# Kernel optimization log

Hardware: AMD Instinct MI355X
Metric: run time of the kernel (lower is better)

The kernel has to match this reference:

```python
import jax, jax.numpy as jnp
import numpy as np

EPS = 1e-5
NUM_HEADS = 4


def setup_inputs() -> dict:
    key = jax.random.key(0)
    ks = jax.random.split(key, 6)
    B, C, H, W = 16, 256, 32, 32
    x = jax.random.normal(ks[0], (B, C, H, W), dtype=jnp.float32)
    gamma = jnp.ones((C,), jnp.float32)
    beta = jnp.zeros((C,), jnp.float32)
    run_mean = jax.random.normal(ks[1], (C,), dtype=jnp.float32) * 0.1
    run_var = jax.random.uniform(ks[2], (C,), dtype=jnp.float32, minval=0.5, maxval=1.5)
    qkv_w = jax.random.normal(ks[3], (3 * C, C), dtype=jnp.float32) * (1.0 / np.sqrt(C))
    qkv_b = jnp.zeros((3 * C,), jnp.float32)
    out_w = jax.random.normal(ks[4], (C, C), dtype=jnp.float32) * (1.0 / np.sqrt(C))
    out_b = jnp.zeros((C,), jnp.float32)
    return {"x": x, "gamma": gamma, "beta": beta, "run_mean": run_mean,
            "run_var": run_var, "qkv_w": qkv_w, "qkv_b": qkv_b,
            "out_w": out_w, "out_b": out_b}


def reference(x, gamma, beta, run_mean, run_var, qkv_w, qkv_b, out_w, out_b):
    B, C, H, W = x.shape
    n = NUM_HEADS
    hd = C // n
    # BatchNorm2d (eval mode, running stats)
    inv = jax.lax.rsqrt(run_var + EPS)
    xn = (x - run_mean[:, None, None]) * (inv * gamma)[:, None, None] + beta[:, None, None]
    # 1x1 conv -> QKV: [B, 3C, H, W]
    qkv = jnp.einsum('oc,bchw->bohw', qkv_w, xn) + qkv_b[:, None, None]
    qkv = qkv.reshape(B, n, 3 * hd, H, W)
    q, k, v = qkv[:, :, :hd], qkv[:, :, hd:2 * hd], qkv[:, :, 2 * hd:]
    # full spatial attention; note scale is sqrt(C), per source
    attn = jnp.einsum('bnchw,bncyx->bnhwyx', q, k) / jnp.sqrt(jnp.float32(C))
    attn = jax.nn.softmax(attn.reshape(B, n, H, W, H * W), axis=-1)
    attn = attn.reshape(B, n, H, W, H, W)
    av = jnp.einsum('bnhwyx,bncyx->bnchw', attn, v).reshape(B, C, H, W)
    out = jnp.einsum('oc,bchw->bohw', out_w, av) + out_b[:, None, None]
    return x + out
```

## Files before the change

kernel.cpp:

```cpp
#include <hip/hip_runtime.h>
#include <hip/hip_bf16.h>

__device__ __forceinline__ float bf2f(unsigned short u) {
    return __uint_as_float(((unsigned int)u) << 16);
}
__device__ __forceinline__ unsigned short f2bf(float f) {
    unsigned int u = __float_as_uint(f);
    unsigned int r = (u + 0x7fffu + ((u >> 16) & 1u)) >> 16;
    return (unsigned short)r;
}
__device__ __forceinline__ float ld1(const void* p, long i, bool isf32) {
    return isf32 ? ((const float*)p)[i] : bf2f(((const unsigned short*)p)[i]);
}

typedef __attribute__((ext_vector_type(8))) short bh8;
typedef __attribute__((ext_vector_type(4))) float f32x4;

#define S_TOK 1024
#define C_DIM 256
#define O_QKV 768
#define HD    64
#define NREG  196608
#define QOFF  0
#define KOFF  65536
#define VOFF  131072

__global__ __launch_bounds__(256) void prep_kernel(
    const void* __restrict__ gamma, const void* __restrict__ beta,
    const void* __restrict__ rmean, const void* __restrict__ rvar,
    const void* __restrict__ qkv_w, const void* __restrict__ qkv_b,
    const void* __restrict__ out_w, const void* __restrict__ out_b,
    const void* __restrict__ x,
    unsigned short* __restrict__ w1b, float* __restrict__ b1,
    unsigned short* __restrict__ w2b, float* __restrict__ b2,
    unsigned short* __restrict__ xT, int* __restrict__ flg)
{
    const unsigned g0 = *(const unsigned*)gamma;
    const bool isf32 = (g0 == 0x3F800000u);
    const int t   = threadIdx.x;
    const int blk = blockIdx.x;
    if (blk == 0 && t == 0) flg[0] = isf32 ? 1 : 0;
    if (blk < O_QKV) {
        const int c = t, o = blk;
        const float v  = ld1(rvar, c, isf32);
        const float a  = ld1(gamma, c, isf32) * rsqrtf(fmaxf(v, 0.f) + 1e-5f);
        const float sh = ld1(beta, c, isf32) - ld1(rmean, c, isf32) * a;
        const float w  = ld1(qkv_w, (long)o * C_DIM + c, isf32);
        w1b[(size_t)o * C_DIM + c] = f2bf(w * a);
        __shared__ float red[256];
        red[c] = w * sh;
        __syncthreads();
        for (int st = 128; st > 0; st >>= 1) {
            if (c < st) red[c] += red[c + st];
            __syncthreads();
        }
        if (c == 0) b1[o] = ld1(qkv_b, o, isf32) + red[0];
    } else if (blk < 1024) {
        const int c = t, o = blk - O_QKV;
        w2b[(size_t)o * C_DIM + c] = f2bf(ld1(out_w, (long)o * C_DIM + c, isf32));
        if (c == 0) b2[o] = ld1(out_b, o, isf32);
    } else {
        const int idx = blk - 1024;
        const int b   = idx >> 6;
        const int s0  = (idx & 15) * 64;
        const int c0  = ((idx >> 4) & 3) * 64;
        __shared__ unsigned short ts[64 * 66];
        const int wave = t >> 6, lane = t & 63;
#pragma unroll
        for (int it = 0; it < 16; ++it) {
            const int ci = it * 4 + wave;
            const float v = ld1(x, ((size_t)b * C_DIM + c0 + ci) * S_TOK + s0 + lane, isf32);
            ts[lane * 66 + ci] = f2bf(v);
        }
        __syncthreads();
        const int tok = t >> 2, cq = t & 3;
        const uint4 a0 = *(const uint4*)&ts[tok * 66 + cq * 16];
        const uint4 a1 = *(const uint4*)&ts[tok * 66 + cq * 16 + 8];
        unsigned short* dst = xT + (((size_t)b << 10) + s0 + tok) * C_DIM + c0 + cq * 16;
        *(uint4*)dst = a0;
        *(uint4*)(dst + 8) = a1;
    }
}

__global__ __launch_bounds__(256) void gemm_qkv_kernel(
    const unsigned short* __restrict__ w1b, const float* __restrict__ b1,
    const unsigned short* __restrict__ xT, unsigned short* __restrict__ qkv,
    int b0)
{
    const int s0 = blockIdx.x * 64;
    const int o0 = blockIdx.y * 64;
    const int z  = blockIdx.z;
    const int b  = b0 + z;
    const int t  = threadIdx.x;
    const int wave = t >> 6, lane = t & 63;
    const int quad = lane >> 4, l16 = lane & 15;

    __shared__ unsigned short xs[64 * 258];

    const unsigned short* xb = xT + (((size_t)b << 10) + s0) * C_DIM;
#pragma unroll
    for (int it = 0; it < 8; ++it) {
        const int idx = it * 256 + t;
        const int tok = idx >> 5, c = (idx & 31) * 8;
        const bh8 v = *(const bh8*)&xb[tok * C_DIM + c];
        const ushort4* vp = (const ushort4*)&v;
        *(ushort4*)&xs[tok * 258 + c]     = vp[0];
        *(ushort4*)&xs[tok * 258 + c + 4] = vp[1];
    }
    const int ow = o0 + wave * 16 + l16;
    bh8 af[8];
#pragma unroll
    for (int kc = 0; kc < 8; ++kc)
        af[kc] = *(const bh8*)&w1b[(size_t)ow * C_DIM + kc * 32 + quad * 8];
    __syncthreads();

    f32x4 acc[4];
#pragma unroll
    for (int nt = 0; nt < 4; ++nt) acc[nt] = (f32x4){0.f, 0.f, 0.f, 0.f};
#pragma unroll
    for (int kc = 0; kc < 8; ++kc) {
#pragma unroll
        for (int nt = 0; nt < 4; ++nt) {
            const bh8 bf = *(const bh8*)&xs[(nt * 16 + l16) * 258 + kc * 32 + quad * 8];
            acc[nt] = __builtin_amdgcn_mfma_f32_16x16x32_bf16(af[kc], bf, acc[nt], 0, 0, 0);
        }
    }
    const int n      = o0 / 192;
    const int region = (o0 >> 6) % 3;
    const int och    = wave * 16 + quad * 4;
    float bias_r[4];
#pragma unroll
    for (int r = 0; r < 4; ++r) bias_r[r] = b1[o0 + och + r];
    unsigned short* hb = qkv + (size_t)z * O_QKV * S_TOK + n * NREG;
    if (region < 2) {
        const float sc = (region == 0) ? 0.0625f : 1.0f;
        unsigned short* qb = hb + (region == 0 ? QOFF : KOFF);
#pragma unroll
        for (int nt = 0; nt < 4; ++nt) {
            const int tk = s0 + nt * 16 + l16;
            ushort4 rr;
            rr.x = f2bf((acc[nt][0] + bias_r[0]) * sc);
            rr.y = f2bf((acc[nt][1] + bias_r[1]) * sc);
            rr.z = f2bf((acc[nt][2] + bias_r[2]) * sc);
            rr.w = f2bf((acc[nt][3] + bias_r[3]) * sc);
            *(ushort4*)&qb[(size_t)tk * 64 + och] = rr;
        }
    } else {
        unsigned short* vb = hb + VOFF;
#pragma unroll
        for (int nt = 0; nt < 4; ++nt) {
            const int tk = s0 + nt * 16 + l16;
#pragma unroll
            for (int r = 0; r < 4; ++r)
                vb[(size_t)(och + r) * S_TOK + tk] = f2bf(acc[nt][r] + bias_r[r]);
        }
    }
}

__global__ __launch_bounds__(256, 4) void attn_mfma_kernel(
    const unsigned short* __restrict__ qkv, unsigned short* __restrict__ avT)
{
    const int n  = blockIdx.x & 3;
    const int z  = blockIdx.x >> 2;
    const int qt = blockIdx.y;
    const int q0 = qt * 64;
    const int t  = threadIdx.x;
    const int wave = t >> 6, lane = t & 63;
    const int quad = lane >> 4, l16 = lane & 15;

    const unsigned short* qtp = qkv + (size_t)z * O_QKV * S_TOK + n * NREG + QOFF;
    const unsigned short* ktp = qtp + KOFF;
    const unsigned short* vcp = qtp + VOFF;

    __shared__ unsigned short p_lds[64 * 72];
    __shared__ float rs_lds[64 * 4];

    bh8 qf[4][2];
#pragma unroll
    for (int qs = 0; qs < 4; ++qs) {
        const size_t qrow = (size_t)(q0 + qs * 16 + l16) * 64;
        qf[qs][0] = *(const bh8*)&qtp[qrow + quad * 8];
        qf[qs][1] = *(const bh8*)&qtp[qrow + 32 + quad * 8];
    }

    f32x4 oacc[4];
#pragma unroll
    for (int i = 0; i < 4; ++i) oacc[i] = (f32x4){0.f, 0.f, 0.f, 0.f};
    float rs[4][4];
#pragma unroll
    for (int qs = 0; qs < 4; ++qs)
#pragma unroll
        for (int r = 0; r < 4; ++r) rs[qs][r] = 0.f;

    for (int chunk = 0; chunk < 16; ++chunk) {
        const int c0 = chunk * 64;
        const size_t krow = (size_t)(c0 + wave * 16 + l16) * 64;
        const bh8 kf0 = *(const bh8*)&ktp[krow + quad * 8];
        const bh8 kf1 = *(const bh8*)&ktp[krow + 32 + quad * 8];
        const size_t vrow = (size_t)(wave * 16 + l16) * S_TOK + c0;
        const bh8 vf0 = *(const bh8*)&vcp[vrow + quad * 8];
        const bh8 vf1 = *(const bh8*)&vcp[vrow + 32 + quad * 8];

        f32x4 sacc[4];
#pragma unroll
        for (int qs = 0; qs < 4; ++qs) {
            f32x4 a = (f32x4){0.f, 0.f, 0.f, 0.f};
            a = __builtin_amdgcn_mfma_f32_16x16x32_bf16(qf[qs][0], kf0, a, 0, 0, 0);
            a = __builtin_amdgcn_mfma_f32_16x16x32_bf16(qf[qs][1], kf1, a, 0, 0, 0);
            sacc[qs] = a;
        }
        __syncthreads();
#pragma unroll
        for (int qs = 0; qs < 4; ++qs) {
#pragma unroll
            for (int r = 0; r < 4; ++r) {
                const float p = __expf(sacc[qs][r] - 8.0f);
                rs[qs][r] += p;
                p_lds[(qs * 16 + quad * 4 + r) * 72 + wave * 16 + l16] =
                    (unsigned short)(__float_as_uint(p) >> 16);
            }
        }
        __syncthreads();
#pragma unroll
        for (int qs = 0; qs < 4; ++qs) {
            const bh8 pf0 = *(const bh8*)&p_lds[(qs * 16 + l16) * 72 + quad * 8];
            const bh8 pf1 = *(const bh8*)&p_lds[(qs * 16 + l16) * 72 + 32 + quad * 8];
            oacc[qs] = __builtin_amdgcn_mfma_f32_16x16x32_bf16(pf0, vf0, oacc[qs], 0, 0, 0);
            oacc[qs] = __builtin_amdgcn_mfma_f32_16x16x32_bf16(pf1, vf1, oacc[qs], 0, 0, 0);
        }
    }
#pragma unroll
    for (int off = 1; off < 16; off <<= 1) {
#pragma unroll
        for (int qs = 0; qs < 4; ++qs)
#pragma unroll
            for (int r = 0; r < 4; ++r) rs[qs][r] += __shfl_xor(rs[qs][r], off);
    }
    if (l16 == 0) {
#pragma unroll
        for (int qs = 0; qs < 4; ++qs)
#pragma unroll
            for (int r = 0; r < 4; ++r)
                rs_lds[(qs * 16 + quad * 4 + r) * 4 + wave] = rs[qs][r];
    }
    __syncthreads();
    const int ch = wave * 16 + l16;
#pragma unroll
    for (int qs = 0; qs < 4; ++qs) {
#pragma unroll
        for (int r = 0; r < 4; ++r) {
            const int q = qs * 16 + quad * 4 + r;
            const float4 rw = *(const float4*)&rs_lds[q * 4];
            const float inv = 1.0f / (rw.x + rw.y + rw.z + rw.w);
            p_lds[q * 72 + ch] = f2bf(oacc[qs][r] * inv);
        }
    }
    __syncthreads();
    const int tok = t >> 2, cq = t & 3;
    const uint4 w0 = *(const uint4*)&p_lds[tok * 72 + cq * 16];
    const uint4 w1 = *(const uint4*)&p_lds[tok * 72 + cq * 16 + 8];
    unsigned short* dst = avT + (((size_t)z << 10) + q0 + tok) * C_DIM + n * HD + cq * 16;
    *(uint4*)dst = w0;
    *(uint4*)(dst + 8) = w1;
}

__global__ __launch_bounds__(256) void gemm_out_kernel(
    const unsigned short* __restrict__ w2b, const float* __restrict__ b2,
    const void* __restrict__ x, const unsigned short* __restrict__ avT,
    void* __restrict__ out, int b0, const int* __restrict__ flg)
{
    const bool isf32 = (flg[0] != 0);
    const int s0 = blockIdx.x * 64;
    const int o0 = blockIdx.y * 64;
    const int z  = blockIdx.z;
    const int b  = b0 + z;
    const int t  = threadIdx.x;
    const int wave = t >> 6, lane = t & 63;
    const int quad = lane >> 4, l16 = lane & 15;

    __shared__ unsigned short vs_lds[64 * 258];

    const unsigned short* ab = avT + (((size_t)z << 10) + s0) * C_DIM;
#pragma unroll
    for (int it = 0; it < 8; ++it) {
        const int idx = it * 256 + t;
        const int tok = idx >> 5, c = (idx & 31) * 8;
        const bh8 v = *(const bh8*)&ab[tok * C_DIM + c];
        const ushort4* vp = (const ushort4*)&v;
        *(ushort4*)&vs_lds[tok * 258 + c]     = vp[0];
        *(ushort4*)&vs_lds[tok * 258 + c + 4] = vp[1];
    }
    const int ow = o0 + wave * 16 + l16;
    bh8 af[8];
#pragma unroll
    for (int kc = 0; kc < 8; ++kc)
        af[kc] = *(const bh8*)&w2b[(size_t)ow * C_DIM + kc * 32 + quad * 8];
    __syncthreads();

    f32x4 acc[4];
#pragma unroll
    for (int nt = 0; nt < 4; ++nt) acc[nt] = (f32x4){0.f, 0.f, 0.f, 0.f};
#pragma unroll
    for (int kc = 0; kc < 8; ++kc) {
#pragma unroll
        for (int nt = 0; nt < 4; ++nt) {
            const bh8 bf = *(const bh8*)&vs_lds[(nt * 16 + l16) * 258 + kc * 32 + quad * 8];
            acc[nt] = __builtin_amdgcn_mfma_f32_16x16x32_bf16(af[kc], bf, acc[nt], 0, 0, 0);
        }
    }
    const int obase = o0 + wave * 16 + quad * 4;
    float bias_r[4];
#pragma unroll
    for (int r = 0; r < 4; ++r) bias_r[r] = b2[obase + r];
#pragma unroll
    for (int nt = 0; nt < 4; ++nt) {
        const int tk = s0 + nt * 16 + l16;
#pragma unroll
        for (int r = 0; r < 4; ++r) {
            const size_t base = ((size_t)b * C_DIM + obase + r) * S_TOK + tk;
            if (isf32) {
                ((float*)out)[base] = acc[nt][r] + bias_r[r] + ((const float*)x)[base];
            } else {
                ((unsigned short*)out)[base] =
                    f2bf(acc[nt][r] + bias_r[r] + bf2f(((const unsigned short*)x)[base]));
            }
        }
    }
}

extern "C" void kernel_launch(void* const* d_in, const int* in_sizes, int n_in,
                              void* d_out, int out_size, void* d_ws, size_t ws_size,
                              hipStream_t stream)
{
    const void* x     = d_in[0];
    const void* gamma = d_in[1];
    const void* beta  = d_in[2];
    const void* rmean = d_in[3];
    const void* rvar  = d_in[4];
    const void* qkv_w = d_in[5];
    const void* qkv_b = d_in[6];
    const void* out_w = d_in[7];
    const void* out_b = d_in[8];

    unsigned short* w1b = (unsigned short*)d_ws;
    unsigned short* w2b = w1b + 768 * 256;
    float* b1 = (float*)(w2b + 256 * 256);
    float* b2 = b1 + 768;
    int*   flg = (int*)(b2 + 256);
    unsigned short* xT = (unsigned short*)(flg + 4);
    const size_t fixed_bytes = (768 * 256 + 256 * 256) * 2 + (768 + 256) * 4 + 16
                             + (size_t)16 * 1024 * 256 * 2;
    const size_t per_b = (size_t)(768 * 1024 + 256 * 1024) * 2;

    long long avail = (long long)ws_size - (long long)fixed_bytes;
    int G = (avail > 0) ? (int)(avail / (long long)per_b) : 1;
    if (G < 1) G = 1;
    if (G > 16) G = 16;

    unsigned short* qkv = (unsigned short*)((char*)d_ws + fixed_bytes);
    unsigned short* avT = qkv + (size_t)G * 768 * 1024;

    prep_kernel<<<2048, 256, 0, stream>>>(gamma, beta, rmean, rvar, qkv_w, qkv_b,
                                          out_w, out_b, x, w1b, b1, w2b, b2, xT, flg);
    for (int b0 = 0; b0 < 16; b0 += G) {
        const int gb = (16 - b0 < G) ? (16 - b0) : G;
        gemm_qkv_kernel<<<dim3(16, 12, gb), 256, 0, stream>>>(w1b, b1, xT, qkv, b0);
        attn_mfma_kernel<<<dim3(4 * gb, 16, 1), 256, 0, stream>>>(qkv, avT);
        gemm_out_kernel<<<dim3(16, 4, gb), 256, 0, stream>>>(w2b, b2, x, avT, d_out, b0, flg);
    }
}
```

Before: 162.6 us.

## Fuse x transpose/convert into QKV GEMM and reuse staged tile across output tiles

Removes the separate transpose of x into a bf16 token-major buffer from the prep kernel. The QKV GEMM now loads x directly, converts and transposes it into shared memory itself. Each block then loops over six 64-wide output tiles, so every staged x tile is reused instead of being reloaded twelve times. The trade-off is far fewer GEMM blocks (grid y drops from 12 to 2), which serializes work per block and may lower occupancy. Uncoalesced 2-byte LDS writes during staging could also slow it, and G is forced to an even value.

```diff
diff --git a/kernel.cpp b/kernel.cpp
--- a/kernel.cpp
+++ b/kernel.cpp
@@ -15,6 +15,8 @@
 
 typedef __attribute__((ext_vector_type(8))) short bh8;
 typedef __attribute__((ext_vector_type(4))) float f32x4;
+
+#define MFMA(a, b, c) __builtin_amdgcn_mfma_f32_16x16x32_bf16(a, b, c, 0, 0, 0)
 
 #define S_TOK 1024
 #define C_DIM 256
@@ -30,10 +32,9 @@
     const void* __restrict__ rmean, const void* __restrict__ rvar,
     const void* __restrict__ qkv_w, const void* __restrict__ qkv_b,
     const void* __restrict__ out_w, const void* __restrict__ out_b,
-    const void* __restrict__ x,
     unsigned short* __restrict__ w1b, float* __restrict__ b1,
     unsigned short* __restrict__ w2b, float* __restrict__ b2,
-    unsigned short* __restrict__ xT, int* __restrict__ flg)
+    int* __restrict__ flg)
 {
     const unsigned g0 = *(const unsigned*)gamma;
     const bool isf32 = (g0 == 0x3F800000u);
@@ -55,104 +56,87 @@
             __syncthreads();
         }
         if (c == 0) b1[o] = ld1(qkv_b, o, isf32) + red[0];
-    } else if (blk < 1024) {
+    } else {
         const int c = t, o = blk - O_QKV;
         w2b[(size_t)o * C_DIM + c] = f2bf(ld1(out_w, (long)o * C_DIM + c, isf32));
         if (c == 0) b2[o] = ld1(out_b, o, isf32);
-    } else {
-        const int idx = blk - 1024;
-        const int b   = idx >> 6;
-        const int s0  = (idx & 15) * 64;
-        const int c0  = ((idx >> 4) & 3) * 64;
-        __shared__ unsigned short ts[64 * 66];
-        const int wave = t >> 6, lane = t & 63;
-#pragma unroll
-        for (int it = 0; it < 16; ++it) {
-            const int ci = it * 4 + wave;
-            const float v = ld1(x, ((size_t)b * C_DIM + c0 + ci) * S_TOK + s0 + lane, isf32);
-            ts[lane * 66 + ci] = f2bf(v);
-        }
-        __syncthreads();
-        const int tok = t >> 2, cq = t & 3;
-        const uint4 a0 = *(const uint4*)&ts[tok * 66 + cq * 16];
-        const uint4 a1 = *(const uint4*)&ts[tok * 66 + cq * 16 + 8];
-        unsigned short* dst = xT + (((size_t)b << 10) + s0 + tok) * C_DIM + c0 + cq * 16;
-        *(uint4*)dst = a0;
-        *(uint4*)(dst + 8) = a1;
     }
 }
 
 __global__ __launch_bounds__(256) void gemm_qkv_kernel(
     const unsigned short* __restrict__ w1b, const float* __restrict__ b1,
-    const unsigned short* __restrict__ xT, unsigned short* __restrict__ qkv,
-    int b0)
-{
+    const void* __restrict__ x, unsigned short* __restrict__ qkv,
+    int b0, const int* __restrict__ flg)
+{
+    const bool isf32 = (flg[0] != 0);
     const int s0 = blockIdx.x * 64;
-    const int o0 = blockIdx.y * 64;
+    const int oh = blockIdx.y;
     const int z  = blockIdx.z;
     const int b  = b0 + z;
     const int t  = threadIdx.x;
     const int wave = t >> 6, lane = t & 63;
     const int quad = lane >> 4, l16 = lane & 15;
 
-    __shared__ unsigned short xs[64 * 258];
-
-    const unsigned short* xb = xT + (((size_t)b << 10) + s0) * C_DIM;
-#pragma unroll
-    for (int it = 0; it < 8; ++it) {
-        const int idx = it * 256 + t;
-        const int tok = idx >> 5, c = (idx & 31) * 8;
-        const bh8 v = *(const bh8*)&xb[tok * C_DIM + c];
-        const ushort4* vp = (const ushort4*)&v;
-        *(ushort4*)&xs[tok * 258 + c]     = vp[0];
-        *(ushort4*)&xs[tok * 258 + c + 4] = vp[1];
-    }
-    const int ow = o0 + wave * 16 + l16;
-    bh8 af[8];
-#pragma unroll
-    for (int kc = 0; kc < 8; ++kc)
-        af[kc] = *(const bh8*)&w1b[(size_t)ow * C_DIM + kc * 32 + quad * 8];
+    __shared__ unsigned short xs[64 * 266];
+
+    const size_t xbase = (size_t)b * C_DIM * S_TOK + s0 + lane;
+#pragma unroll 4
+    for (int it = 0; it < 64; ++it) {
+        const int ci = it * 4 + wave;
+        const float v = ld1(x, xbase + (size_t)ci * S_TOK, isf32);
+        xs[lane * 266 + ci] = f2bf(v);
+    }
     __syncthreads();
 
-    f32x4 acc[4];
-#pragma unroll
-    for (int nt = 0; nt < 4; ++nt) acc[nt] = (f32x4){0.f, 0.f, 0.f, 0.f};
-#pragma unroll
-    for (int kc = 0; kc < 8; ++kc) {
-#pragma unroll
-        for (int nt = 0; nt < 4; ++nt) {
-            const bh8 bf = *(const bh8*)&xs[(nt * 16 + l16) * 258 + kc * 32 + quad * 8];
-            acc[nt] = __builtin_amdgcn_mfma_f32_16x16x32_bf16(af[kc], bf, acc[nt], 0, 0, 0);
-        }
-    }
-    const int n      = o0 / 192;
-    const int region = (o0 >> 6) % 3;
-    const int och    = wave * 16 + quad * 4;
-    float bias_r[4];
-#pragma unroll
-    for (int r = 0; r < 4; ++r) bias_r[r] = b1[o0 + och + r];
-    unsigned short* hb = qkv + (size_t)z * O_QKV * S_TOK + n * NREG;
-    if (region < 2) {
-        const float sc = (region == 0) ? 0.0625f : 1.0f;
-        unsigned short* qb = hb + (region == 0 ? QOFF : KOFF);
-#pragma unroll
-        for (int nt = 0; nt < 4; ++nt) {
-            const int tk = s0 + nt * 16 + l16;
-            ushort4 rr;
-            rr.x = f2bf((acc[nt][0] + bias_r[0]) * sc);
-            rr.y = f2bf((acc[nt][1] + bias_r[1]) * sc);
-            rr.z = f2bf((acc[nt][2] + bias_r[2]) * sc);
-            rr.w = f2bf((acc[nt][3] + bias_r[3]) * sc);
-            *(ushort4*)&qb[(size_t)tk * 64 + och] = rr;
-        }
-    } else {
-        unsigned short* vb = hb + VOFF;
-#pragma unroll
-        for (int nt = 0; nt < 4; ++nt) {
-            const int tk = s0 + nt * 16 + l16;
-#pragma unroll
-            for (int r = 0; r < 4; ++r)
-                vb[(size_t)(och + r) * S_TOK + tk] = f2bf(acc[nt][r] + bias_r[r]);
+#pragma unroll 1
+    for (int ot = 0; ot < 6; ++ot) {
+        const int o0 = (oh * 6 + ot) * 64;
+        const int ow = o0 + wave * 16 + l16;
+        bh8 af[8];
+#pragma unroll
+        for (int kc = 0; kc < 8; ++kc)
+            af[kc] = *(const bh8*)&w1b[(size_t)ow * C_DIM + kc * 32 + quad * 8];
+
+        f32x4 acc[4];
+#pragma unroll
+        for (int nt = 0; nt < 4; ++nt) acc[nt] = (f32x4){0.f, 0.f, 0.f, 0.f};
+#pragma unroll
+        for (int kc = 0; kc < 8; ++kc) {
+#pragma unroll
+            for (int nt = 0; nt < 4; ++nt) {
+                const bh8 bf = *(const bh8*)&xs[(nt * 16 + l16) * 266 + kc * 32 + quad * 8];
+                acc[nt] = MFMA(af[kc], bf, acc[nt]);
+            }
+        }
+        const int n      = o0 / 192;
+        const int region = (o0 >> 6) % 3;
+        const int och    = wave * 16 + quad * 4;
+        float bias_r[4];
+#pragma unroll
+        for (int r = 0; r < 4; ++r) bias_r[r] = b1[o0 + och + r];
+        unsigned short* hb = qkv + (size_t)z * O_QKV * S_TOK + n * NREG;
+        if (region < 2) {
+            const float sc = (region == 0) ? 0.0625f : 1.0f;
+            unsigned short* qb = hb + (region == 0 ? QOFF : KOFF);
+#pragma unroll
+            for (int nt = 0; nt < 4; ++nt) {
+                const int tk = s0 + nt * 16 + l16;
+                ushort4 rr;
+                rr.x = f2bf((acc[nt][0] + bias_r[0]) * sc);
+                rr.y = f2bf((acc[nt][1] + bias_r[1]) * sc);
+                rr.z = f2bf((acc[nt][2] + bias_r[2]) * sc);
+                rr.w = f2bf((acc[nt][3] + bias_r[3]) * sc);
+                *(ushort4*)&qb[(size_t)tk * 64 + och] = rr;
+            }
+        } else {
+            unsigned short* vb = hb + VOFF;
+#pragma unroll
+            for (int nt = 0; nt < 4; ++nt) {
+                const int tk = s0 + nt * 16 + l16;
+#pragma unroll
+                for (int r = 0; r < 4; ++r)
+                    vb[(size_t)(och + r) * S_TOK + tk] = f2bf(acc[nt][r] + bias_r[r]);
+            }
         }
     }
 }
@@ -205,8 +189,8 @@
 #pragma unroll
         for (int qs = 0; qs < 4; ++qs) {
             f32x4 a = (f32x4){0.f, 0.f, 0.f, 0.f};
-            a = __builtin_amdgcn_mfma_f32_16x16x32_bf16(qf[qs][0], kf0, a, 0, 0, 0);
-            a = __builtin_amdgcn_mfma_f32_16x16x32_bf16(qf[qs][1], kf1, a, 0, 0, 0);
+            a = MFMA(qf[qs][0], kf0, a);
+            a = MFMA(qf[qs][1], kf1, a);
             sacc[qs] = a;
         }
         __syncthreads();
@@ -225,8 +209,8 @@
         for (int qs = 0; qs < 4; ++qs) {
             const bh8 pf0 = *(const bh8*)&p_lds[(qs * 16 + l16) * 72 + quad * 8];
             const bh8 pf1 = *(const bh8*)&p_lds[(qs * 16 + l16) * 72 + 32 + quad * 8];
-            oacc[qs] = __builtin_amdgcn_mfma_f32_16x16x32_bf16(pf0, vf0, oacc[qs], 0, 0, 0);
-            oacc[qs] = __builtin_amdgcn_mfma_f32_16x16x32_bf16(pf1, vf1, oacc[qs], 0, 0, 0);
+            oacc[qs] = MFMA(pf0, vf0, oacc[qs]);
+            oacc[qs] = MFMA(pf1, vf1, oacc[qs]);
         }
     }
 #pragma unroll
@@ -305,7 +289,7 @@
 #pragma unroll
         for (int nt = 0; nt < 4; ++nt) {
             const bh8 bf = *(const bh8*)&vs_lds[(nt * 16 + l16) * 258 + kc * 32 + quad * 8];
-            acc[nt] = __builtin_amdgcn_mfma_f32_16x16x32_bf16(af[kc], bf, acc[nt], 0, 0, 0);
+            acc[nt] = MFMA(af[kc], bf, acc[nt]);
         }
     }
     const int obase = o0 + wave * 16 + quad * 4;
@@ -347,24 +331,23 @@
     float* b1 = (float*)(w2b + 256 * 256);
     float* b2 = b1 + 768;
     int*   flg = (int*)(b2 + 256);
-    unsigned short* xT = (unsigned short*)(flg + 4);
-    const size_t fixed_bytes = (768 * 256 + 256 * 256) * 2 + (768 + 256) * 4 + 16
-                             + (size_t)16 * 1024 * 256 * 2;
+    const size_t fixed_bytes = (768 * 256 + 256 * 256) * 2 + (768 + 256) * 4 + 16;
     const size_t per_b = (size_t)(768 * 1024 + 256 * 1024) * 2;
 
     long long avail = (long long)ws_size - (long long)fixed_bytes;
     int G = (avail > 0) ? (int)(avail / (long long)per_b) : 1;
     if (G < 1) G = 1;
     if (G > 16) G = 16;
+    if (G > 1) G &= ~1;
 
     unsigned short* qkv = (unsigned short*)((char*)d_ws + fixed_bytes);
     unsigned short* avT = qkv + (size_t)G * 768 * 1024;
 
-    prep_kernel<<<2048, 256, 0, stream>>>(gamma, beta, rmean, rvar, qkv_w, qkv_b,
-                                          out_w, out_b, x, w1b, b1, w2b, b2, xT, flg);
+    prep_kernel<<<1024, 256, 0, stream>>>(gamma, beta, rmean, rvar, qkv_w, qkv_b,
+                                          out_w, out_b, w1b, b1, w2b, b2, flg);
     for (int b0 = 0; b0 < 16; b0 += G) {
         const int gb = (16 - b0 < G) ? (16 - b0) : G;
-        gemm_qkv_kernel<<<dim3(16, 12, gb), 256, 0, stream>>>(w1b, b1, xT, qkv, b0);
+        gemm_qkv_kernel<<<dim3(16, 2, gb), 256, 0, stream>>>(w1b, b1, x, qkv, b0, flg);
         attn_mfma_kernel<<<dim3(4 * gb, 16, 1), 256, 0, stream>>>(qkv, avT);
         gemm_out_kernel<<<dim3(16, 4, gb), 256, 0, stream>>>(w2b, b2, x, avT, d_out, b0, flg);
     }
```

After: 172.1 us. 1.06x slower.
